# Kernel optimization log

Measured on AMD Instinct MI355X. Metric: run time of the kernel, lower is better.

## Reference

```python
import jax, jax.numpy as jnp
import numpy as np
from jax import lax

CONF_THR = 0.1
IOU_THR = 0.45
B, C, IMG = 4, 20, 416.0
SIZES = {"p3": 8112, "p4": 2028, "p5": 507}


def setup_inputs() -> dict:
    key = jax.random.key(0)
    ks = jax.random.split(key, 4 * len(SIZES))
    d = {}
    i = 0
    for name, n in SIZES.items():
        # valid xyxy boxes: random centers in image, widths/heights in [4, 104]
        cxy = jax.random.uniform(ks[i], (B, n, 2), jnp.float32) * IMG
        wh = jax.random.uniform(ks[i + 1], (B, n, 2), jnp.float32) * 100.0 + 4.0
        d[f"{name}_boxes"] = jnp.concatenate([cxy - wh / 2, cxy + wh / 2], axis=-1)
        d[f"{name}_conf"] = jax.random.uniform(ks[i + 2], (B, n, 1), jnp.float32)
        d[f"{name}_cls"] = jax.random.uniform(ks[i + 3], (B, n, C), jnp.float32)
        i += 4
    return d


def _iou_row(b, boxes, area_b, areas):
    # IoU of one box b [4] against all boxes [N,4] (same clamp math as torch _nms)
    xx1 = jnp.maximum(boxes[:, 0], b[0])
    yy1 = jnp.maximum(boxes[:, 1], b[1])
    xx2 = jnp.minimum(boxes[:, 2], b[2])
    yy2 = jnp.minimum(boxes[:, 3], b[3])
    inter = jnp.maximum(xx2 - xx1, 0.0) * jnp.maximum(yy2 - yy1, 0.0)
    return inter / (area_b + areas - inter)


def _nms_keep(boxes, scores, valid):
    # Greedy NMS on one image with padding. Returns (order, keep) so that
    # boxes[order][keep] matches torch's detections[keep-indices] set.
    n = boxes.shape[0]
    order = jnp.argsort(-scores)  # descending, as scores.sort(descending=True)
    sb = boxes[order]
    sv = valid[order]
    areas = (sb[:, 2] - sb[:, 0]) * (sb[:, 3] - sb[:, 1])
    idx = jnp.arange(n)

    def body(i, supp):
        keep_i = jnp.logical_and(sv[i], jnp.logical_not(supp[i]))
        iou = _iou_row(sb[i], sb, areas[i], areas)  # [N]
        return jnp.logical_or(supp, keep_i & (iou > IOU_THR) & (idx > i))

    supp = lax.fori_loop(0, n, body, jnp.zeros(n, bool))
    keep = jnp.logical_and(sv, jnp.logical_not(supp))
    return order, keep


def reference(p3_boxes, p3_conf, p3_cls, p4_boxes, p4_conf, p4_cls,
              p5_boxes, p5_conf, p5_cls):
    boxes = jnp.concatenate([p3_boxes, p4_boxes, p5_boxes], axis=1)   # [B,N,4]
    conf = jnp.concatenate([p3_conf, p4_conf, p5_conf], axis=1)[..., 0]  # [B,N]
    cls = jnp.concatenate([p3_cls, p4_cls, p5_cls], axis=1)           # [B,N,C]

    cls_conf = jnp.max(cls, axis=-1)
    cls_idx = jnp.argmax(cls, axis=-1)
    valid = conf > CONF_THR           # torch drops these; we mask (padded NMS)
    score = jnp.where(valid, conf * cls_conf, 0.0)

    order, keep = jax.vmap(_nms_keep)(boxes, score, valid)  # [B,N] each

    sb = jnp.take_along_axis(boxes, order[..., None], axis=1)
    ss = jnp.take_along_axis(score, order, axis=1)
    sc = jnp.take_along_axis(cls_idx, order, axis=1)
    out_score = jnp.where(keep, ss, 0.0)
    dets = jnp.concatenate(
        [sb, out_score[..., None], sc.astype(jnp.float32)[..., None]], axis=-1
    )  # [B,N,6] = (x1,y1,x2,y2,conf,class), score-sorted; keep marks survivors
    return dets, keep
```

## Files before the change

### kernel.cpp

```cpp
#include <hip/hip_runtime.h>
#include <stdint.h>

#define NB3 8112
#define NB4 2028
#define NB5 507
#define NTOT 10647
#define NBATCH 4
#define NCLS 20
#define NW32 333
#define NW64 167
#define NPAIR 84
#define NTAIL 23
#define RCH 11
#define RSL 6
#define RTP 7
#define LDS_CAP 9984
#define CONF_THR_F 0.1f
#define IOU_THR_F 0.45f
#define IOU_MID ((double)IOU_THR_F + 0x1p-26)

typedef unsigned long long u64;

__global__ void prep_kernel(const float* __restrict__ p3b, const float* __restrict__ p3c, const float* __restrict__ p3k,
                            const float* __restrict__ p4b, const float* __restrict__ p4c, const float* __restrict__ p4k,
                            const float* __restrict__ p5b, const float* __restrict__ p5c, const float* __restrict__ p5k,
                            uint64_t* __restrict__ keys, float4* __restrict__ boxes_cat,
                            float* __restrict__ score, int* __restrict__ clsidx, uint32_t* __restrict__ svout,
                            int* __restrict__ nvalid, int* __restrict__ rank)
{
#pragma clang fp contract(off)
    int idx = blockIdx.x * 256 + threadIdx.x;
    if (idx < NBATCH) nvalid[idx] = 0;
    if (idx >= NBATCH * NTOT) return;
    rank[idx] = 0;
    int b = idx / NTOT;
    int i = idx - b * NTOT;

    const float* bx; const float* cf; const float* cl; int n, off;
    if (i < NB3)            { bx = p3b; cf = p3c; cl = p3k; n = NB3; off = i; }
    else if (i < NB3 + NB4) { bx = p4b; cf = p4c; cl = p4k; n = NB4; off = i - NB3; }
    else                    { bx = p5b; cf = p5c; cl = p5k; n = NB5; off = i - NB3 - NB4; }

    size_t e = (size_t)b * n + off;
    float4 box = *(const float4*)(bx + e * 4);
    float conf = cf[e];
    const float* c = cl + e * NCLS;
    float m = c[0]; int mi = 0;
    #pragma unroll
    for (int k = 1; k < NCLS; ++k) { float v = c[k]; if (v > m) { m = v; mi = k; } }

    bool valid = conf > CONF_THR_F;
    float s = valid ? conf * m : 0.0f;
    uint32_t sb = __float_as_uint(s);
    keys[idx]      = ((uint64_t)sb << 32) | (uint32_t)(0xFFFFFFFFu - (uint32_t)i);
    boxes_cat[idx] = box;
    score[idx]     = s;
    clsidx[idx]    = mi;
    svout[idx]     = valid ? 1u : 0u;
}

__global__ void __launch_bounds__(256) rank_partial(const uint64_t* __restrict__ keys,
                                                    int* __restrict__ rank)
{
    int b = blockIdx.z;
    const uint64_t* kb = keys + (size_t)b * NTOT;
    int i0 = blockIdx.x * 1024 + threadIdx.x;
    uint64_t k0 = (i0       < NTOT) ? kb[i0]       : 0ull;
    uint64_t k1 = (i0 + 256 < NTOT) ? kb[i0 + 256] : 0ull;
    uint64_t k2 = (i0 + 512 < NTOT) ? kb[i0 + 512] : 0ull;
    uint64_t k3 = (i0 + 768 < NTOT) ? kb[i0 + 768] : 0ull;
    int r0 = 0, r1 = 0, r2 = 0, r3 = 0;

    __shared__ uint64_t tile[256];
    for (int tt = 0; tt < RTP; ++tt) {
        int j = (blockIdx.y * RTP + tt) * 256 + threadIdx.x;
        tile[threadIdx.x] = (j < NTOT) ? kb[j] : 0ull;
        __syncthreads();
        #pragma unroll 8
        for (int t = 0; t < 256; ++t) {
            uint64_t kt = tile[t];
            r0 += (kt > k0) ? 1 : 0;
            r1 += (kt > k1) ? 1 : 0;
            r2 += (kt > k2) ? 1 : 0;
            r3 += (kt > k3) ? 1 : 0;
        }
        __syncthreads();
    }

    int* rb = rank + (size_t)b * NTOT;
    if (i0       < NTOT) atomicAdd(&rb[i0],       r0);
    if (i0 + 256 < NTOT) atomicAdd(&rb[i0 + 256], r1);
    if (i0 + 512 < NTOT) atomicAdd(&rb[i0 + 512], r2);
    if (i0 + 768 < NTOT) atomicAdd(&rb[i0 + 768], r3);
}

__global__ void inv_kernel(const int* __restrict__ rank, int* __restrict__ inv)
{
    int idx = blockIdx.x * 256 + threadIdx.x;
    if (idx >= NBATCH * NTOT) return;
    int b = idx / NTOT;
    int i = idx - b * NTOT;
    inv[(size_t)b * NTOT + rank[idx]] = i;
}

__global__ void gather_kernel(const int* __restrict__ inv,
                              const float4* __restrict__ boxes_cat,
                              const float* __restrict__ score,
                              const int* __restrict__ clsidx,
                              const uint32_t* __restrict__ sv,
                              float4* __restrict__ sboxes, float* __restrict__ sscore,
                              int* __restrict__ scls, uint32_t* __restrict__ ssv,
                              int* __restrict__ nvalid, int need_nvalid)
{
    int idx = blockIdx.x * 256 + threadIdx.x;
    if (idx >= NBATCH * NTOT) return;
    int b = idx / NTOT;
    int i = idx - b * NTOT;
    size_t base = (size_t)b * NTOT;
    int src = inv[idx];
    float4 box = boxes_cat[base + src];
    uint32_t v = sv[base + src];
    sboxes[idx] = box;
    sscore[idx] = score[base + src];
    scls[idx]   = clsidx[base + src];
    ssv[idx]    = v;
    if (need_nvalid) {
        int mv = v ? (i + 1) : 0;
        #pragma unroll
        for (int d = 32; d >= 1; d >>= 1) {
            int o = __shfl_xor(mv, d, 64);
            mv = (o > mv) ? o : mv;
        }
        if ((threadIdx.x & 63) == 0 && mv > 0) atomicMax(&nvalid[b], mv);
    }
}

__global__ void __launch_bounds__(256) mask_build(const float4* __restrict__ sboxes,
                                                  u64* __restrict__ mask,
                                                  u64* __restrict__ ldiag,
                                                  u64* __restrict__ s1diag,
                                                  u64* __restrict__ s2diag,
                                                  u64* __restrict__ s3diag,
                                                  u64* __restrict__ s4diag,
                                                  u64* __restrict__ s5diag,
                                                  u64* __restrict__ lt1)
{
#pragma clang fp contract(off)
    int c = blockIdx.y;
    if (c < blockIdx.x * 4) return;
    int b = blockIdx.z;
    int sub = threadIdx.x >> 6;
    int lane = threadIdx.x & 63;
    int r = blockIdx.x * 4 + sub;

    __shared__ float4 cb[64];
    __shared__ float  ca[64];
    if (threadIdx.x < 64) {
        int j = c * 64 + threadIdx.x;
        float4 bj = sboxes[(size_t)b * NTOT + (j < NTOT ? j : NTOT - 1)];
        cb[threadIdx.x] = bj;
        ca[threadIdx.x] = (bj.z - bj.x) * (bj.w - bj.y);
    }
    __syncthreads();

    if (r >= NW64 || c < r) return;
    int i = r * 64 + lane;
    float4 bi = sboxes[(size_t)b * NTOT + (i < NTOT ? i : NTOT - 1)];
    float ax1 = bi.x, ay1 = bi.y, ax2 = bi.z, ay2 = bi.w;
    float area_i = (ax2 - ax1) * (ay2 - ay1);

    u64 hh = 0;
    #pragma unroll 8
    for (int k = 0; k < 64; ++k) {
        float4 bj = cb[k];
        float xx1 = fmaxf(bj.x, ax1);
        float yy1 = fmaxf(bj.y, ay1);
        float xx2 = fminf(bj.z, ax2);
        float yy2 = fminf(bj.w, ay2);
        float w = fmaxf(xx2 - xx1, 0.0f);
        float h = fmaxf(yy2 - yy1, 0.0f);
        float inter = w * h;
        float uni = (area_i + ca[k]) - inter;
        bool hit = (double)inter > IOU_MID * (double)uni;
        hh |= (u64)hit << k;
    }

    u64 colmask = (c == NW64 - 1) ? ((1ull << NTAIL) - 1) : ~0ull;
    u64 mw = hh & colmask;

    if (i < NTOT) {
        size_t bl = ((size_t)b * NW64 + r) * 64 + lane;
        if (c == r) {
            u64 gtmask = (lane < 63) ? (~0ull << (lane + 1)) : 0ull;
            mask[((size_t)b * NTOT + i) * NW64 + c] = mw & gtmask;
            ldiag[bl] = hh & ((1ull << lane) - 1);
        } else {
            mask[((size_t)b * NTOT + i) * NW64 + c] = mw;
            if (c == r + 1) s1diag[bl] = mw;
            if (c == r + 2) s2diag[bl] = mw;
            if (c == r + 3) s3diag[bl] = mw;
            if (c == r + 4) s4diag[bl] = mw;
            if (c == r + 5) s5diag[bl] = mw;
        }
    }
    if (c == r + 1 && (r & 1) == 0) {
        u64 ltw = 0;
        #pragma unroll 8
        for (int k = 0; k < 64; ++k) {
            u64 bw = __ballot((mw >> k) & 1ull);
            if (lane == k) ltw = bw;
        }
        lt1[((size_t)b * NPAIR + (r >> 1)) * 64 + lane] = ltw;
    }
}

static __device__ __forceinline__ void bar_sync()
{
    asm volatile("s_waitcnt lgkmcnt(0)" ::: "memory");
    __builtin_amdgcn_s_barrier();
    asm volatile("" ::: "memory");
}

static __device__ __forceinline__ u64 rfl64(u64 x)
{
    uint32_t lo = __builtin_amdgcn_readfirstlane((uint32_t)x);
    uint32_t hi = __builtin_amdgcn_readfirstlane((uint32_t)(x >> 32));
    return ((u64)hi << 32) | (u64)lo;
}

__global__ void __launch_bounds__(1024) resolve_kernel(const u64* __restrict__ mask,
                                                       const u64* __restrict__ ldiag,
                                                       const u64* __restrict__ s1diag,
                                                       const u64* __restrict__ s2diag,
                                                       const u64* __restrict__ s3diag,
                                                       const u64* __restrict__ s4diag,
                                                       const u64* __restrict__ s5diag,
                                                       const u64* __restrict__ lt1,
                                                       const float4* __restrict__ sboxes,
                                                       const float* __restrict__ sscore,
                                                       const int* __restrict__ scls,
                                                       const uint32_t* __restrict__ ssv,
                                                       u64* __restrict__ rem_out,
                                                       float* __restrict__ out)
{
    int b = blockIdx.x;
    int tid = threadIdx.x;
    int lane = tid & 63;
    int wv = tid >> 6;
    const u64* M   = mask   + (size_t)b * NTOT * NW64;
    const u64* LD  = ldiag  + (size_t)b * NW64 * 64;
    const u64* S1A = s1diag + (size_t)b * NW64 * 64;
    const u64* S2A = s2diag + (size_t)b * NW64 * 64;
    const u64* S3A = s3diag + (size_t)b * NW64 * 64;
    const u64* S4A = s4diag + (size_t)b * NW64 * 64;
    const u64* S5A = s5diag + (size_t)b * NW64 * 64;
    const u64* LT  = lt1    + (size_t)b * NPAIR * 64;

    __shared__ u64 rem_s[NW64 + 1];
    __shared__ u64 v_s[NW64 + 1];
    __shared__ u64 kept_s[2][2];
    __shared__ int klist[2][128];

    for (int t = tid; t < NW64 + 1; t += 1024) rem_s[t] = 0ull;
    for (int t = wv; t < NW64; t += 16) {
        int i = t * 64 + lane;
        uint32_t v = (i < NTOT) ? ssv[(size_t)b * NTOT + i] : 0u;
        u64 w = __ballot(v != 0u);
        if (lane == 0) v_s[t] = w;
    }
    if (tid == 0) {
        v_s[NW64] = 0ull;
        kept_s[0][0] = kept_s[0][1] = kept_s[1][0] = kept_s[1][1] = 0ull;
        klist[0][0] = 0; klist[1][0] = 0;
    }

    u64 ld0 = 0, ld1 = 0, lt = 0;
    u64 s1_0 = 0, s2_0 = 0, s3_0 = 0, s4_0 = 0, s5_0 = 0;
    u64 s1_1 = 0, s2_1 = 0, s3_1 = 0, s4_1 = 0;
    if (wv == 0) {
        ld0 = LD[lane];      ld1 = LD[64 + lane];   lt = LT[lane];
        s1_0 = S1A[lane]; s2_0 = S2A[lane]; s3_0 = S3A[lane];
        s4_0 = S4A[lane]; s5_0 = S5A[lane];
        s1_1 = S1A[64 + lane]; s2_1 = S2A[64 + lane];
        s3_1 = S3A[64 + lane]; s4_1 = S4A[64 + lane];
    }

    u64 df[5][3];
    #pragma unroll
    for (int t = 0; t < 5; ++t) {
        #pragma unroll
        for (int c = 0; c < 3; ++c) df[t][c] = 0ull;
    }

    bar_sync();

    for (int p = 0; p < NPAIR; ++p) {
        int par = p & 1;
        int w0 = 2 * p, w1 = 2 * p + 1;

        if (wv == 0) {
            int pn = (p + 1 < NPAIR) ? p + 1 : p;
            int i0 = 2 * pn;
            int i1 = (2 * pn + 1 < NW64) ? 2 * pn + 1 : NW64 - 1;
            u64 nld0 = LD [(size_t)i0 * 64 + lane];
            u64 nld1 = LD [(size_t)i1 * 64 + lane];
            u64 nlt  = LT [(size_t)pn * 64 + lane];
            u64 ns1_0 = S1A[(size_t)i0 * 64 + lane];
            u64 ns2_0 = S2A[(size_t)i0 * 64 + lane];
            u64 ns3_0 = S3A[(size_t)i0 * 64 + lane];
            u64 ns4_0 = S4A[(size_t)i0 * 64 + lane];
            u64 ns5_0 = S5A[(size_t)i0 * 64 + lane];
            u64 ns1_1 = S1A[(size_t)i1 * 64 + lane];
            u64 ns2_1 = S2A[(size_t)i1 * 64 + lane];
            u64 ns3_1 = S3A[(size_t)i1 * 64 + lane];
            u64 ns4_1 = S4A[(size_t)i1 * 64 + lane];

            u64 a0 = rfl64(v_s[w0] & ~rem_s[w0]);
            u64 a1 = rfl64(v_s[w1] & ~rem_s[w1]);
            u64 U0 = a0, U1 = a1, K0 = 0, K1 = 0;
            while (U0 | U1) {
                u64 UK0 = U0 | K0, UK1 = U1 | K1;
                bool in0 = (U0 >> lane) & 1;
                bool in1 = (U1 >> lane) & 1;
                u64 nk0 = __ballot(in0 && (ld0 & UK0) == 0ull);
                u64 nk1 = __ballot(in1 && ((lt & UK0) | (ld1 & UK1)) == 0ull);
                u64 nr0 = __ballot(in0 && (ld0 & K0) != 0ull);
                u64 nr1 = __ballot(in1 && ((lt & K0) | (ld1 & K1)) != 0ull);
                K0 |= nk0; K1 |= nk1;
                U0 &= ~(nk0 | nr0); U1 &= ~(nk1 | nr1);
            }

            if (lane == 0) {
                kept_s[par][0] = K0; kept_s[par][1] = K1;
                u64 sup0 = a0 & ~K0;
                u64 sup1 = a1 & ~K1;
                if (sup0) rem_s[w0] |= sup0;
                if (sup1) rem_s[w1] |= sup1;
            }
            int w2 = w0 + 2, w3 = w0 + 3, w4 = w0 + 4, w5 = w0 + 5;
            bool h2 = w2 < NW64, h3 = w3 < NW64, h4 = w4 < NW64, h5 = w5 < NW64;
            if ((K0 >> lane) & 1) {
                if (h2 && s2_0) atomicOr((unsigned long long*)&rem_s[w2], (unsigned long long)s2_0);
                if (h3 && s3_0) atomicOr((unsigned long long*)&rem_s[w3], (unsigned long long)s3_0);
                if (h4 && s4_0) atomicOr((unsigned long long*)&rem_s[w4], (unsigned long long)s4_0);
                if (h5 && s5_0) atomicOr((unsigned long long*)&rem_s[w5], (unsigned long long)s5_0);
            }
            if ((K1 >> lane) & 1) {
                if (h2 && s1_1) atomicOr((unsigned long long*)&rem_s[w2], (unsigned long long)s1_1);
                if (h3 && s2_1) atomicOr((unsigned long long*)&rem_s[w3], (unsigned long long)s2_1);
                if (h4 && s3_1) atomicOr((unsigned long long*)&rem_s[w4], (unsigned long long)s3_1);
                if (h5 && s4_1) atomicOr((unsigned long long*)&rem_s[w5], (unsigned long long)s4_1);
            }
            ld0 = nld0; ld1 = nld1; lt = nlt;
            s1_0 = ns1_0; s2_0 = ns2_0; s3_0 = ns3_0; s4_0 = ns4_0; s5_0 = ns5_0;
            s1_1 = ns1_1; s2_1 = ns2_1; s3_1 = ns3_1; s4_1 = ns4_1;
        } else {
            int parw = par ^ 1;
            u64 k0 = kept_s[parw][0], k1 = kept_s[parw][1];
            int n0 = __popcll(k0);
            int nk = n0 + __popcll(k1);
            u64 below = (1ull << lane) - 1;
            if ((k0 >> lane) & 1) klist[parw][__popcll(k0 & below)] = lane;
            if ((k1 >> lane) & 1) klist[parw][n0 + __popcll(k1 & below)] = 64 + lane;

            #pragma unroll
            for (int t = 0; t < 5; ++t) {
                #pragma unroll
                for (int c = 0; c < 3; ++c) {
                    if (df[t][c])
                        atomicOr((unsigned long long*)&rem_s[2 * p + 2 + (c << 6) + lane],
                                 (unsigned long long)df[t][c]);
                }
            }

            int q = (p > 0) ? p - 1 : 0;
            int nkc = (nk < 64) ? nk : 64;
            #pragma unroll
            for (int t = 0; t < 5; ++t) {
                int s = (wv - 1) + t * 15;
                bool has = (p > 0) && (s < nkc);
                int rr = klist[parw][has ? s : 0];
                const u64* R = M + (size_t)(q * 128 + rr) * NW64;
                #pragma unroll
                for (int c = 0; c < 3; ++c) {
                    int w = 2 * q + 6 + (c << 6) + lane;
                    df[t][c] = (has && w < NW64) ? R[w] : 0ull;
                }
            }
            for (int base = 64; base < nk; base += 64) {
                #pragma unroll
                for (int t = 0; t < 5; ++t) {
                    int s = base + (wv - 1) + t * 15;
                    bool has = s < nk;
                    int rr = klist[parw][has ? s : 0];
                    const u64* R = M + (size_t)(q * 128 + rr) * NW64;
                    #pragma unroll
                    for (int c = 0; c < 3; ++c) {
                        int w = 2 * q + 6 + (c << 6) + lane;
                        u64 v2 = (has && w < NW64) ? R[w] : 0ull;
                        if (v2) atomicOr((unsigned long long*)&rem_s[w], (unsigned long long)v2);
                    }
                }
            }
        }

        bar_sync();
    }


    for (int t = tid; t < NW64; t += 1024)
        rem_out[(size_t)b * NW64 + t] = rem_s[t];

    for (int t = tid; t < NTOT; t += 1024) {
        size_t idx = (size_t)b * NTOT + t;
        float4 box = sboxes[idx];
        u64 rw = rem_s[t >> 6];
        bool keep = (ssv[idx] != 0u) && !((rw >> (t & 63)) & 1ull);
        float sc = keep ? sscore[idx] : 0.0f;
        float* d = out + idx * 6;
        d[0] = box.x; d[1] = box.y; d[2] = box.z; d[3] = box.w;
        d[4] = sc;    d[5] = (float)scls[idx];
        out[(size_t)NBATCH * NTOT * 6 + idx] = keep ? 1.0f : 0.0f;
    }
}

extern __shared__ unsigned char nms_smem[];

__global__ void __launch_bounds__(1024) nms_kernel(const float4* __restrict__ sboxes,
                                                   const uint32_t* __restrict__ ssv,
                                                   const int* __restrict__ nvalid_arr,
                                                   uint32_t* __restrict__ supp_out)
{
#pragma clang fp contract(off)
    int b = blockIdx.x;
    float4*   lbox = (float4*)nms_smem;
    uint32_t* supp = (uint32_t*)(nms_smem + (size_t)LDS_CAP * 16);
    uint32_t* svb  = supp + NW32;

    int nv = nvalid_arr[b];
    const float4* gb = sboxes + (size_t)b * NTOT;
    const uint32_t* gv = ssv + (size_t)b * NTOT;

    for (int t = threadIdx.x; t < NW32; t += 1024) { supp[t] = 0u; svb[t] = 0u; }
    __syncthreads();
    for (int t = threadIdx.x; t < nv; t += 1024) {
        if (t < LDS_CAP) lbox[t] = gb[t];
        if (gv[t]) atomicOr(&svb[t >> 5], 1u << (t & 31));
    }
    __syncthreads();

    for (int i = 0; i < nv; ++i) {
        uint32_t sw = supp[i >> 5];
        if ((sw >> (i & 31)) & 1u) continue;
        uint32_t vw = svb[i >> 5];
        if (!((vw >> (i & 31)) & 1u)) continue;

        float4 bi = (i < LDS_CAP) ? lbox[i] : gb[i];
        float ax1 = bi.x, ay1 = bi.y, ax2 = bi.z, ay2 = bi.w;
        float area_i = (ax2 - ax1) * (ay2 - ay1);

        for (int j = i + 1 + (int)threadIdx.x; j < nv; j += 1024) {
            float4 bj = (j < LDS_CAP) ? lbox[j] : gb[j];
            float xx1 = fmaxf(bj.x, ax1);
            float yy1 = fmaxf(bj.y, ay1);
            float xx2 = fminf(bj.z, ax2);
            float yy2 = fminf(bj.w, ay2);
            float w = fmaxf(xx2 - xx1, 0.0f);
            float h = fmaxf(yy2 - yy1, 0.0f);
            float inter  = w * h;
            float area_j = (bj.z - bj.x) * (bj.w - bj.y);
            float iou = inter / ((area_i + area_j) - inter);
            if (iou > IOU_THR_F) atomicOr(&supp[j >> 5], 1u << (j & 31));
        }
        __syncthreads();
    }

    __syncthreads();
    for (int t = threadIdx.x; t < NW32; t += 1024)
        supp_out[(size_t)b * (2 * NW64) + t] = supp[t];
}

__global__ void out_kernel(const float4* __restrict__ sboxes, const float* __restrict__ sscore,
                           const int* __restrict__ scls, const uint32_t* __restrict__ ssv,
                           const u64* __restrict__ rem, float* __restrict__ out)
{
    int idx = blockIdx.x * 256 + threadIdx.x;
    if (idx >= NBATCH * NTOT) return;
    int b = idx / NTOT;
    int p = idx - b * NTOT;

    float4 box = sboxes[idx];
    u64 rw = rem[(size_t)b * NW64 + (p >> 6)];
    bool keep = (ssv[idx] != 0u) && !((rw >> (p & 63)) & 1ull);
    float sc = keep ? sscore[idx] : 0.0f;

    float* d = out + (size_t)idx * 6;
    d[0] = box.x; d[1] = box.y; d[2] = box.z; d[3] = box.w;
    d[4] = sc;    d[5] = (float)scls[idx];
    out[(size_t)NBATCH * NTOT * 6 + idx] = keep ? 1.0f : 0.0f;
}

extern "C" void kernel_launch(void* const* d_in, const int* in_sizes, int n_in,
                              void* d_out, int out_size, void* d_ws, size_t ws_size,
                              hipStream_t stream)
{
    const float* p3b = (const float*)d_in[0];
    const float* p3c = (const float*)d_in[1];
    const float* p3k = (const float*)d_in[2];
    const float* p4b = (const float*)d_in[3];
    const float* p4c = (const float*)d_in[4];
    const float* p4k = (const float*)d_in[5];
    const float* p5b = (const float*)d_in[6];
    const float* p5c = (const float*)d_in[7];
    const float* p5k = (const float*)d_in[8];
    float* out = (float*)d_out;

    char* ws = (char*)d_ws;
    size_t off = 0;
    auto alloc = [&](size_t bytes) { size_t o = off; off += (bytes + 255) & ~(size_t)255; return o; };
    const size_t BN = (size_t)NBATCH * NTOT;
    uint64_t* keys      = (uint64_t*)(ws + alloc(BN * 8));
    float4*   boxes_cat = (float4*)  (ws + alloc(BN * 16));
    float*    score     = (float*)   (ws + alloc(BN * 4));
    int*      clsidx    = (int*)     (ws + alloc(BN * 4));
    uint32_t* sv        = (uint32_t*)(ws + alloc(BN * 4));
    int*      rank_arr  = (int*)     (ws + alloc(BN * 4));
    int*      inv_arr   = (int*)     (ws + alloc(BN * 4));
    float4*   sboxes    = (float4*)  (ws + alloc(BN * 16));
    float*    sscore    = (float*)   (ws + alloc(BN * 4));
    int*      scls      = (int*)     (ws + alloc(BN * 4));
    uint32_t* ssv       = (uint32_t*)(ws + alloc(BN * 4));
    u64*      rem64     = (u64*)     (ws + alloc((size_t)NBATCH * NW64 * 8));
    int*      nvalid    = (int*)     (ws + alloc(NBATCH * 4));
    u64*      ldiag     = (u64*)     (ws + alloc((size_t)NBATCH * NW64 * 64 * 8));
    u64*      s1diag    = (u64*)     (ws + alloc((size_t)NBATCH * NW64 * 64 * 8));
    u64*      s2diag    = (u64*)     (ws + alloc((size_t)NBATCH * NW64 * 64 * 8));
    u64*      s3diag    = (u64*)     (ws + alloc((size_t)NBATCH * NW64 * 64 * 8));
    u64*      s4diag    = (u64*)     (ws + alloc((size_t)NBATCH * NW64 * 64 * 8));
    u64*      s5diag    = (u64*)     (ws + alloc((size_t)NBATCH * NW64 * 64 * 8));
    u64*      lt1       = (u64*)     (ws + alloc((size_t)NBATCH * NPAIR * 64 * 8));
    u64*      mask      = (u64*)     (ws + alloc((size_t)NBATCH * NTOT * NW64 * 8));
    bool fast = (off <= ws_size);

    int nblk = (int)((BN + 255) / 256);
    prep_kernel<<<nblk, 256, 0, stream>>>(p3b, p3c, p3k, p4b, p4c, p4k, p5b, p5c, p5k,
                                          keys, boxes_cat, score, clsidx, sv,
                                          nvalid, rank_arr);

    dim3 rpgrid(RCH, RSL, NBATCH);
    rank_partial<<<rpgrid, 256, 0, stream>>>(keys, rank_arr);

    inv_kernel<<<nblk, 256, 0, stream>>>(rank_arr, inv_arr);

    gather_kernel<<<nblk, 256, 0, stream>>>(inv_arr, boxes_cat, score, clsidx, sv,
                                            sboxes, sscore, scls, ssv,
                                            nvalid, fast ? 0 : 1);

    if (fast) {
        dim3 mgrid((NW64 + 3) / 4, NW64, NBATCH);
        mask_build<<<mgrid, 256, 0, stream>>>(sboxes, mask, ldiag, s1diag, s2diag,
                                              s3diag, s4diag, s5diag, lt1);
        resolve_kernel<<<NBATCH, 1024, 0, stream>>>(mask, ldiag, s1diag, s2diag, s3diag,
                                                    s4diag, s5diag, lt1,
                                                    sboxes, sscore, scls, ssv,
                                                    rem64, out);
    } else {
        hipMemsetAsync(rem64, 0, (size_t)NBATCH * NW64 * 8, stream);
        size_t smem = (size_t)LDS_CAP * 16 + (size_t)NW32 * 4 * 2;
        smem = (smem + 15) & ~(size_t)15;
        hipFuncSetAttribute((const void*)nms_kernel, hipFuncAttributeMaxDynamicSharedMemorySize, (int)smem);
        nms_kernel<<<NBATCH, 1024, smem, stream>>>(sboxes, ssv, nvalid, (uint32_t*)rem64);
        out_kernel<<<nblk, 256, 0, stream>>>(sboxes, sscore, scls, ssv, rem64, out);
    }
}
```

Baseline: 432.0 us.

## Offload far-diagonal suppression from leader wave and shrink resolve block to 512

The resolve kernel drops from 1024 to 512 threads, and the remaining helper waves each take 8 kept rows instead of 5. The suppression ORs for diagonal offsets 4 and 5 move off the serial leader wave (wave 0) onto wave 1, which applies them one pair late using the kept masks from the previous step. The intent is to shorten the leader's critical path per pair and cut barrier cost with fewer waves, at the price of more registers per helper thread and a deferred update that must still land before those words are read. The rank kernel also reads its LDS tile as 128-bit pairs to halve the number of LDS loads.

```diff
diff --git a/kernel.cpp b/kernel.cpp
--- a/kernel.cpp
+++ b/kernel.cpp
@@ -71,18 +71,19 @@
     uint64_t k3 = (i0 + 768 < NTOT) ? kb[i0 + 768] : 0ull;
     int r0 = 0, r1 = 0, r2 = 0, r3 = 0;
 
-    __shared__ uint64_t tile[256];
+    __shared__ ulonglong2 tile2[128];
+    uint64_t* tile = (uint64_t*)tile2;
     for (int tt = 0; tt < RTP; ++tt) {
         int j = (blockIdx.y * RTP + tt) * 256 + threadIdx.x;
         tile[threadIdx.x] = (j < NTOT) ? kb[j] : 0ull;
         __syncthreads();
-        #pragma unroll 8
-        for (int t = 0; t < 256; ++t) {
-            uint64_t kt = tile[t];
-            r0 += (kt > k0) ? 1 : 0;
-            r1 += (kt > k1) ? 1 : 0;
-            r2 += (kt > k2) ? 1 : 0;
-            r3 += (kt > k3) ? 1 : 0;
+        #pragma unroll 4
+        for (int t = 0; t < 128; ++t) {
+            ulonglong2 kt = tile2[t];
+            r0 += ((kt.x > k0) ? 1 : 0) + ((kt.y > k0) ? 1 : 0);
+            r1 += ((kt.x > k1) ? 1 : 0) + ((kt.y > k1) ? 1 : 0);
+            r2 += ((kt.x > k2) ? 1 : 0) + ((kt.y > k2) ? 1 : 0);
+            r3 += ((kt.x > k3) ? 1 : 0) + ((kt.y > k3) ? 1 : 0);
         }
         __syncthreads();
     }
@@ -228,20 +229,20 @@
     return ((u64)hi << 32) | (u64)lo;
 }
 
-__global__ void __launch_bounds__(1024) resolve_kernel(const u64* __restrict__ mask,
-                                                       const u64* __restrict__ ldiag,
-                                                       const u64* __restrict__ s1diag,
-                                                       const u64* __restrict__ s2diag,
-                                                       const u64* __restrict__ s3diag,
-                                                       const u64* __restrict__ s4diag,
-                                                       const u64* __restrict__ s5diag,
-                                                       const u64* __restrict__ lt1,
-                                                       const float4* __restrict__ sboxes,
-                                                       const float* __restrict__ sscore,
-                                                       const int* __restrict__ scls,
-                                                       const uint32_t* __restrict__ ssv,
-                                                       u64* __restrict__ rem_out,
-                                                       float* __restrict__ out)
+__global__ void __launch_bounds__(512) resolve_kernel(const u64* __restrict__ mask,
+                                                      const u64* __restrict__ ldiag,
+                                                      const u64* __restrict__ s1diag,
+                                                      const u64* __restrict__ s2diag,
+                                                      const u64* __restrict__ s3diag,
+                                                      const u64* __restrict__ s4diag,
+                                                      const u64* __restrict__ s5diag,
+                                                      const u64* __restrict__ lt1,
+                                                      const float4* __restrict__ sboxes,
+                                                      const float* __restrict__ sscore,
+                                                      const int* __restrict__ scls,
+                                                      const uint32_t* __restrict__ ssv,
+                                                      u64* __restrict__ rem_out,
+                                                      float* __restrict__ out)
 {
     int b = blockIdx.x;
     int tid = threadIdx.x;
@@ -261,8 +262,8 @@
     __shared__ u64 kept_s[2][2];
     __shared__ int klist[2][128];
 
-    for (int t = tid; t < NW64 + 1; t += 1024) rem_s[t] = 0ull;
-    for (int t = wv; t < NW64; t += 16) {
+    for (int t = tid; t < NW64 + 1; t += 512) rem_s[t] = 0ull;
+    for (int t = wv; t < NW64; t += 8) {
         int i = t * 64 + lane;
         uint32_t v = (i < NTOT) ? ssv[(size_t)b * NTOT + i] : 0u;
         u64 w = __ballot(v != 0u);
@@ -274,20 +275,20 @@
         klist[0][0] = 0; klist[1][0] = 0;
     }
 
-    u64 ld0 = 0, ld1 = 0, lt = 0;
-    u64 s1_0 = 0, s2_0 = 0, s3_0 = 0, s4_0 = 0, s5_0 = 0;
-    u64 s1_1 = 0, s2_1 = 0, s3_1 = 0, s4_1 = 0;
+    u64 ld0 = 0, ld1 = 0, lt = 0, s2_0 = 0, s3_0 = 0, s1_1 = 0, s2_1 = 0;
+    u64 b4_0 = 0, b5_0 = 0, b3_1 = 0, b4_1 = 0;
     if (wv == 0) {
         ld0 = LD[lane];      ld1 = LD[64 + lane];   lt = LT[lane];
-        s1_0 = S1A[lane]; s2_0 = S2A[lane]; s3_0 = S3A[lane];
-        s4_0 = S4A[lane]; s5_0 = S5A[lane];
+        s2_0 = S2A[lane];    s3_0 = S3A[lane];
         s1_1 = S1A[64 + lane]; s2_1 = S2A[64 + lane];
-        s3_1 = S3A[64 + lane]; s4_1 = S4A[64 + lane];
-    }
-
-    u64 df[5][3];
+    } else if (wv == 1) {
+        b4_0 = S4A[lane];    b5_0 = S5A[lane];
+        b3_1 = S3A[64 + lane]; b4_1 = S4A[64 + lane];
+    }
+
+    u64 df[8][3];
     #pragma unroll
-    for (int t = 0; t < 5; ++t) {
+    for (int t = 0; t < 8; ++t) {
         #pragma unroll
         for (int c = 0; c < 3; ++c) df[t][c] = 0ull;
     }
@@ -305,15 +306,10 @@
             u64 nld0 = LD [(size_t)i0 * 64 + lane];
             u64 nld1 = LD [(size_t)i1 * 64 + lane];
             u64 nlt  = LT [(size_t)pn * 64 + lane];
-            u64 ns1_0 = S1A[(size_t)i0 * 64 + lane];
             u64 ns2_0 = S2A[(size_t)i0 * 64 + lane];
             u64 ns3_0 = S3A[(size_t)i0 * 64 + lane];
-            u64 ns4_0 = S4A[(size_t)i0 * 64 + lane];
-            u64 ns5_0 = S5A[(size_t)i0 * 64 + lane];
             u64 ns1_1 = S1A[(size_t)i1 * 64 + lane];
             u64 ns2_1 = S2A[(size_t)i1 * 64 + lane];
-            u64 ns3_1 = S3A[(size_t)i1 * 64 + lane];
-            u64 ns4_1 = S4A[(size_t)i1 * 64 + lane];
 
             u64 a0 = rfl64(v_s[w0] & ~rem_s[w0]);
             u64 a1 = rfl64(v_s[w1] & ~rem_s[w1]);
@@ -337,23 +333,18 @@
                 if (sup0) rem_s[w0] |= sup0;
                 if (sup1) rem_s[w1] |= sup1;
             }
-            int w2 = w0 + 2, w3 = w0 + 3, w4 = w0 + 4, w5 = w0 + 5;
-            bool h2 = w2 < NW64, h3 = w3 < NW64, h4 = w4 < NW64, h5 = w5 < NW64;
+            int w2 = w0 + 2, w3 = w0 + 3;
+            bool h2 = w2 < NW64, h3 = w3 < NW64;
             if ((K0 >> lane) & 1) {
                 if (h2 && s2_0) atomicOr((unsigned long long*)&rem_s[w2], (unsigned long long)s2_0);
                 if (h3 && s3_0) atomicOr((unsigned long long*)&rem_s[w3], (unsigned long long)s3_0);
-                if (h4 && s4_0) atomicOr((unsigned long long*)&rem_s[w4], (unsigned long long)s4_0);
-                if (h5 && s5_0) atomicOr((unsigned long long*)&rem_s[w5], (unsigned long long)s5_0);
             }
             if ((K1 >> lane) & 1) {
                 if (h2 && s1_1) atomicOr((unsigned long long*)&rem_s[w2], (unsigned long long)s1_1);
                 if (h3 && s2_1) atomicOr((unsigned long long*)&rem_s[w3], (unsigned long long)s2_1);
-                if (h4 && s3_1) atomicOr((unsigned long long*)&rem_s[w4], (unsigned long long)s3_1);
-                if (h5 && s4_1) atomicOr((unsigned long long*)&rem_s[w5], (unsigned long long)s4_1);
             }
             ld0 = nld0; ld1 = nld1; lt = nlt;
-            s1_0 = ns1_0; s2_0 = ns2_0; s3_0 = ns3_0; s4_0 = ns4_0; s5_0 = ns5_0;
-            s1_1 = ns1_1; s2_1 = ns2_1; s3_1 = ns3_1; s4_1 = ns4_1;
+            s2_0 = ns2_0; s3_0 = ns3_0; s1_1 = ns1_1; s2_1 = ns2_1;
         } else {
             int parw = par ^ 1;
             u64 k0 = kept_s[parw][0], k1 = kept_s[parw][1];
@@ -363,8 +354,29 @@
             if ((k0 >> lane) & 1) klist[parw][__popcll(k0 & below)] = lane;
             if ((k1 >> lane) & 1) klist[parw][n0 + __popcll(k1 & below)] = 64 + lane;
 
+            if (wv == 1) {
+                if (p > 0) {
+                    int t2 = 2 * p + 2, t3 = 2 * p + 3;
+                    bool g2 = t2 < NW64, g3 = t3 < NW64;
+                    if ((k0 >> lane) & 1) {
+                        if (g2 && b4_0) atomicOr((unsigned long long*)&rem_s[t2], (unsigned long long)b4_0);
+                        if (g3 && b5_0) atomicOr((unsigned long long*)&rem_s[t3], (unsigned long long)b5_0);
+                    }
+                    if ((k1 >> lane) & 1) {
+                        if (g2 && b3_1) atomicOr((unsigned long long*)&rem_s[t2], (unsigned long long)b3_1);
+                        if (g3 && b4_1) atomicOr((unsigned long long*)&rem_s[t3], (unsigned long long)b4_1);
+                    }
+                }
+                int i0 = 2 * p;
+                int i1 = (2 * p + 1 < NW64) ? 2 * p + 1 : NW64 - 1;
+                b4_0 = S4A[(size_t)i0 * 64 + lane];
+                b5_0 = S5A[(size_t)i0 * 64 + lane];
+                b3_1 = S3A[(size_t)i1 * 64 + lane];
+                b4_1 = S4A[(size_t)i1 * 64 + lane];
+            }
+
             #pragma unroll
-            for (int t = 0; t < 5; ++t) {
+            for (int t = 0; t < 8; ++t) {
                 #pragma unroll
                 for (int c = 0; c < 3; ++c) {
                     if (df[t][c])
@@ -374,10 +386,10 @@
             }
 
             int q = (p > 0) ? p - 1 : 0;
-            int nkc = (nk < 64) ? nk : 64;
+            int nkc = (nk < 56) ? nk : 56;
             #pragma unroll
-            for (int t = 0; t < 5; ++t) {
-                int s = (wv - 1) + t * 15;
+            for (int t = 0; t < 8; ++t) {
+                int s = (wv - 1) + t * 7;
                 bool has = (p > 0) && (s < nkc);
                 int rr = klist[parw][has ? s : 0];
                 const u64* R = M + (size_t)(q * 128 + rr) * NW64;
@@ -387,10 +399,10 @@
                     df[t][c] = (has && w < NW64) ? R[w] : 0ull;
                 }
             }
-            for (int base = 64; base < nk; base += 64) {
+            for (int base = 56; base < nk; base += 56) {
                 #pragma unroll
-                for (int t = 0; t < 5; ++t) {
-                    int s = base + (wv - 1) + t * 15;
+                for (int t = 0; t < 8; ++t) {
+                    int s = base + (wv - 1) + t * 7;
                     bool has = s < nk;
                     int rr = klist[parw][has ? s : 0];
                     const u64* R = M + (size_t)(q * 128 + rr) * NW64;
@@ -408,10 +420,10 @@
     }
 
 
-    for (int t = tid; t < NW64; t += 1024)
+    for (int t = tid; t < NW64; t += 512)
         rem_out[(size_t)b * NW64 + t] = rem_s[t];
 
-    for (int t = tid; t < NTOT; t += 1024) {
+    for (int t = tid; t < NTOT; t += 512) {
         size_t idx = (size_t)b * NTOT + t;
         float4 box = sboxes[idx];
         u64 rw = rem_s[t >> 6];
@@ -560,10 +572,10 @@
         dim3 mgrid((NW64 + 3) / 4, NW64, NBATCH);
         mask_build<<<mgrid, 256, 0, stream>>>(sboxes, mask, ldiag, s1diag, s2diag,
                                               s3diag, s4diag, s5diag, lt1);
-        resolve_kernel<<<NBATCH, 1024, 0, stream>>>(mask, ldiag, s1diag, s2diag, s3diag,
-                                                    s4diag, s5diag, lt1,
-                                                    sboxes, sscore, scls, ssv,
-                                                    rem64, out);
+        resolve_kernel<<<NBATCH, 512, 0, stream>>>(mask, ldiag, s1diag, s2diag, s3diag,
+                                                   s4diag, s5diag, lt1,
+                                                   sboxes, sscore, scls, ssv,
+                                                   rem64, out);
     } else {
         hipMemsetAsync(rem64, 0, (size_t)NBATCH * NW64 * 8, stream);
         size_t smem = (size_t)LDS_CAP * 16 + (size_t)NW32 * 4 * 2;
```

Result: slower. 508.7 us (+17.7%).

## Tile mask_build over 4x4 word blocks and vectorize rank tile reads

Applied to the files above, without the earlier changes.

mask_build now has each block cover four column words (256 boxes staged in LDS) instead of one. This cuts the grid by about four times and reuses each row box across four column tiles, lowering launch, block-scheduling and redundant row-load overhead. rank_partial reads its shared tile as 128-bit pairs to halve the number of LDS loads. Unused s1_0 prefetches are removed from resolve_kernel. The trade-off is more per-thread work and some load imbalance on the diagonal blocks.

```diff
diff --git a/kernel.cpp b/kernel.cpp
--- a/kernel.cpp
+++ b/kernel.cpp
@@ -71,18 +71,19 @@
     uint64_t k3 = (i0 + 768 < NTOT) ? kb[i0 + 768] : 0ull;
     int r0 = 0, r1 = 0, r2 = 0, r3 = 0;
 
-    __shared__ uint64_t tile[256];
+    __shared__ ulonglong2 tile2[128];
+    uint64_t* tile = (uint64_t*)tile2;
     for (int tt = 0; tt < RTP; ++tt) {
         int j = (blockIdx.y * RTP + tt) * 256 + threadIdx.x;
         tile[threadIdx.x] = (j < NTOT) ? kb[j] : 0ull;
         __syncthreads();
-        #pragma unroll 8
-        for (int t = 0; t < 256; ++t) {
-            uint64_t kt = tile[t];
-            r0 += (kt > k0) ? 1 : 0;
-            r1 += (kt > k1) ? 1 : 0;
-            r2 += (kt > k2) ? 1 : 0;
-            r3 += (kt > k3) ? 1 : 0;
+        #pragma unroll 4
+        for (int t = 0; t < 128; ++t) {
+            ulonglong2 kt = tile2[t];
+            r0 += ((kt.x > k0) ? 1 : 0) + ((kt.y > k0) ? 1 : 0);
+            r1 += ((kt.x > k1) ? 1 : 0) + ((kt.y > k1) ? 1 : 0);
+            r2 += ((kt.x > k2) ? 1 : 0) + ((kt.y > k2) ? 1 : 0);
+            r3 += ((kt.x > k3) ? 1 : 0) + ((kt.y > k3) ? 1 : 0);
         }
         __syncthreads();
     }
@@ -146,71 +147,79 @@
                                                   u64* __restrict__ lt1)
 {
 #pragma clang fp contract(off)
-    int c = blockIdx.y;
-    if (c < blockIdx.x * 4) return;
+    int bx = blockIdx.x;
+    int by = blockIdx.y;
+    if (by < bx) return;
     int b = blockIdx.z;
     int sub = threadIdx.x >> 6;
     int lane = threadIdx.x & 63;
-    int r = blockIdx.x * 4 + sub;
-
-    __shared__ float4 cb[64];
-    __shared__ float  ca[64];
-    if (threadIdx.x < 64) {
-        int j = c * 64 + threadIdx.x;
+    int r = bx * 4 + sub;
+
+    __shared__ float4 cb[256];
+    __shared__ float  ca[256];
+    {
+        int j = by * 256 + threadIdx.x;
         float4 bj = sboxes[(size_t)b * NTOT + (j < NTOT ? j : NTOT - 1)];
         cb[threadIdx.x] = bj;
         ca[threadIdx.x] = (bj.z - bj.x) * (bj.w - bj.y);
     }
     __syncthreads();
 
-    if (r >= NW64 || c < r) return;
+    if (r >= NW64) return;
     int i = r * 64 + lane;
-    float4 bi = sboxes[(size_t)b * NTOT + (i < NTOT ? i : NTOT - 1)];
+    bool live = (i < NTOT);
+    float4 bi = sboxes[(size_t)b * NTOT + (live ? i : NTOT - 1)];
     float ax1 = bi.x, ay1 = bi.y, ax2 = bi.z, ay2 = bi.w;
     float area_i = (ax2 - ax1) * (ay2 - ay1);
-
-    u64 hh = 0;
-    #pragma unroll 8
-    for (int k = 0; k < 64; ++k) {
-        float4 bj = cb[k];
-        float xx1 = fmaxf(bj.x, ax1);
-        float yy1 = fmaxf(bj.y, ay1);
-        float xx2 = fminf(bj.z, ax2);
-        float yy2 = fminf(bj.w, ay2);
-        float w = fmaxf(xx2 - xx1, 0.0f);
-        float h = fmaxf(yy2 - yy1, 0.0f);
-        float inter = w * h;
-        float uni = (area_i + ca[k]) - inter;
-        bool hit = (double)inter > IOU_MID * (double)uni;
-        hh |= (u64)hit << k;
-    }
-
-    u64 colmask = (c == NW64 - 1) ? ((1ull << NTAIL) - 1) : ~0ull;
-    u64 mw = hh & colmask;
-
-    if (i < NTOT) {
-        size_t bl = ((size_t)b * NW64 + r) * 64 + lane;
-        if (c == r) {
-            u64 gtmask = (lane < 63) ? (~0ull << (lane + 1)) : 0ull;
-            mask[((size_t)b * NTOT + i) * NW64 + c] = mw & gtmask;
-            ldiag[bl] = hh & ((1ull << lane) - 1);
-        } else {
-            mask[((size_t)b * NTOT + i) * NW64 + c] = mw;
-            if (c == r + 1) s1diag[bl] = mw;
-            if (c == r + 2) s2diag[bl] = mw;
-            if (c == r + 3) s3diag[bl] = mw;
-            if (c == r + 4) s4diag[bl] = mw;
-            if (c == r + 5) s5diag[bl] = mw;
-        }
-    }
-    if (c == r + 1 && (r & 1) == 0) {
-        u64 ltw = 0;
+    size_t bl = ((size_t)b * NW64 + r) * 64 + lane;
+
+    #pragma unroll
+    for (int cc = 0; cc < 4; ++cc) {
+        int c = by * 4 + cc;
+        if (c < r || c >= NW64) continue;
+
+        u64 hh = 0;
         #pragma unroll 8
         for (int k = 0; k < 64; ++k) {
-            u64 bw = __ballot((mw >> k) & 1ull);
-            if (lane == k) ltw = bw;
-        }
-        lt1[((size_t)b * NPAIR + (r >> 1)) * 64 + lane] = ltw;
+            float4 bj = cb[cc * 64 + k];
+            float xx1 = fmaxf(bj.x, ax1);
+            float yy1 = fmaxf(bj.y, ay1);
+            float xx2 = fminf(bj.z, ax2);
+            float yy2 = fminf(bj.w, ay2);
+            float w = fmaxf(xx2 - xx1, 0.0f);
+            float h = fmaxf(yy2 - yy1, 0.0f);
+            float inter = w * h;
+            float uni = (area_i + ca[cc * 64 + k]) - inter;
+            bool hit = (double)inter > IOU_MID * (double)uni;
+            hh |= (u64)hit << k;
+        }
+
+        u64 colmask = (c == NW64 - 1) ? ((1ull << NTAIL) - 1) : ~0ull;
+        u64 mw = hh & colmask;
+
+        if (live) {
+            if (c == r) {
+                u64 gtmask = (lane < 63) ? (~0ull << (lane + 1)) : 0ull;
+                mask[((size_t)b * NTOT + i) * NW64 + c] = mw & gtmask;
+                ldiag[bl] = hh & ((1ull << lane) - 1);
+            } else {
+                mask[((size_t)b * NTOT + i) * NW64 + c] = mw;
+                if (c == r + 1) s1diag[bl] = mw;
+                if (c == r + 2) s2diag[bl] = mw;
+                if (c == r + 3) s3diag[bl] = mw;
+                if (c == r + 4) s4diag[bl] = mw;
+                if (c == r + 5) s5diag[bl] = mw;
+            }
+        }
+        if (c == r + 1 && (r & 1) == 0) {
+            u64 ltw = 0;
+            #pragma unroll 8
+            for (int k = 0; k < 64; ++k) {
+                u64 bw = __ballot((mw >> k) & 1ull);
+                if (lane == k) ltw = bw;
+            }
+            lt1[((size_t)b * NPAIR + (r >> 1)) * 64 + lane] = ltw;
+        }
     }
 }
 
@@ -275,12 +284,11 @@
     }
 
     u64 ld0 = 0, ld1 = 0, lt = 0;
-    u64 s1_0 = 0, s2_0 = 0, s3_0 = 0, s4_0 = 0, s5_0 = 0;
+    u64 s2_0 = 0, s3_0 = 0, s4_0 = 0, s5_0 = 0;
     u64 s1_1 = 0, s2_1 = 0, s3_1 = 0, s4_1 = 0;
     if (wv == 0) {
         ld0 = LD[lane];      ld1 = LD[64 + lane];   lt = LT[lane];
-        s1_0 = S1A[lane]; s2_0 = S2A[lane]; s3_0 = S3A[lane];
-        s4_0 = S4A[lane]; s5_0 = S5A[lane];
+        s2_0 = S2A[lane]; s3_0 = S3A[lane]; s4_0 = S4A[lane]; s5_0 = S5A[lane];
         s1_1 = S1A[64 + lane]; s2_1 = S2A[64 + lane];
         s3_1 = S3A[64 + lane]; s4_1 = S4A[64 + lane];
     }
@@ -305,7 +313,6 @@
             u64 nld0 = LD [(size_t)i0 * 64 + lane];
             u64 nld1 = LD [(size_t)i1 * 64 + lane];
             u64 nlt  = LT [(size_t)pn * 64 + lane];
-            u64 ns1_0 = S1A[(size_t)i0 * 64 + lane];
             u64 ns2_0 = S2A[(size_t)i0 * 64 + lane];
             u64 ns3_0 = S3A[(size_t)i0 * 64 + lane];
             u64 ns4_0 = S4A[(size_t)i0 * 64 + lane];
@@ -352,7 +359,7 @@
                 if (h5 && s4_1) atomicOr((unsigned long long*)&rem_s[w5], (unsigned long long)s4_1);
             }
             ld0 = nld0; ld1 = nld1; lt = nlt;
-            s1_0 = ns1_0; s2_0 = ns2_0; s3_0 = ns3_0; s4_0 = ns4_0; s5_0 = ns5_0;
+            s2_0 = ns2_0; s3_0 = ns3_0; s4_0 = ns4_0; s5_0 = ns5_0;
             s1_1 = ns1_1; s2_1 = ns2_1; s3_1 = ns3_1; s4_1 = ns4_1;
         } else {
             int parw = par ^ 1;
@@ -387,10 +394,10 @@
                     df[t][c] = (has && w < NW64) ? R[w] : 0ull;
                 }
             }
-            for (int base = 64; base < nk; base += 64) {
+            for (int bs = 64; bs < nk; bs += 64) {
                 #pragma unroll
                 for (int t = 0; t < 5; ++t) {
-                    int s = base + (wv - 1) + t * 15;
+                    int s = bs + (wv - 1) + t * 15;
                     bool has = s < nk;
                     int rr = klist[parw][has ? s : 0];
                     const u64* R = M + (size_t)(q * 128 + rr) * NW64;
@@ -557,7 +564,7 @@
                                             nvalid, fast ? 0 : 1);
 
     if (fast) {
-        dim3 mgrid((NW64 + 3) / 4, NW64, NBATCH);
+        dim3 mgrid((NW64 + 3) / 4, (NW64 + 3) / 4, NBATCH);
         mask_build<<<mgrid, 256, 0, stream>>>(sboxes, mask, ldiag, s1diag, s2diag,
                                               s3diag, s4diag, s5diag, lt1);
         resolve_kernel<<<NBATCH, 1024, 0, stream>>>(mask, ldiag, s1diag, s2diag, s3diag,
```

New measurement: 436.9 us. Within noise of the previous version (+1.1%).
